# Kernel optimization log

Hardware: AMD Instinct MI355X
Metric: run time of the kernel (lower is better)

## Reference

```python
import jax, jax.numpy as jnp
import numpy as np

H = 12          # num heads
D = 768         # hidden size
DH = D // H     # size per head
FF = 3072       # intermediate size
EPS = 1e-11


def gelu(x):
    # tanh approximation, matching the TF source exactly
    c = np.sqrt(2.0 / np.pi).astype(np.float32)
    return x * 0.5 * (1.0 + jnp.tanh(c * (x + 0.044715 * jnp.power(x, 3))))


def layer_norm(x, gamma, beta):
    mean = jnp.mean(x, axis=-1, keepdims=True)
    var = jnp.mean(jnp.square(x - mean), axis=-1, keepdims=True)
    return (x - mean) * jax.lax.rsqrt(var + EPS) * gamma + beta


def setup_inputs() -> dict:
    key = jax.random.key(0)
    ks = jax.random.split(key, 12)
    B, S = 16, 512
    std = 0.02
    inp = {
        "x": jax.random.normal(ks[0], (B, S, D), jnp.float32),
        "mask": jnp.ones((B, S), dtype=bool),
        "Wq": jax.random.normal(ks[1], (D, D), jnp.float32) * std,
        "bq": jnp.zeros((D,), jnp.float32),
        "Wk": jax.random.normal(ks[2], (D, D), jnp.float32) * std,
        "bk": jnp.zeros((D,), jnp.float32),
        "Wv": jax.random.normal(ks[3], (D, D), jnp.float32) * std,
        "bv": jnp.zeros((D,), jnp.float32),
        "Wo": jax.random.normal(ks[4], (D, D), jnp.float32) * std,
        "bo": jnp.zeros((D,), jnp.float32),
        "g1": jnp.ones((D,), jnp.float32),
        "b1": jnp.zeros((D,), jnp.float32),
        "Wi": jax.random.normal(ks[5], (D, FF), jnp.float32) * std,
        "bi": jnp.zeros((FF,), jnp.float32),
        "Wo2": jax.random.normal(ks[6], (FF, D), jnp.float32) * std,
        "bo2": jnp.zeros((D,), jnp.float32),
        "g2": jnp.ones((D,), jnp.float32),
        "b2": jnp.zeros((D,), jnp.float32),
    }
    return inp


def reference(x, mask, Wq, bq, Wk, bk, Wv, bv, Wo, bo, g1, b1, Wi, bi, Wo2, bo2, g2, b2):
    B, S, _ = x.shape
    # QKV projections
    q = (x @ Wq + bq).reshape(B, S, H, DH)
    k = (x @ Wk + bk).reshape(B, S, H, DH)
    v = (x @ Wv + bv).reshape(B, S, H, DH)
    # scaled dot-product attention scores [B, H, S, S]
    scores = jnp.einsum("bqhd,bkhd->bhqk", q, k) / np.sqrt(DH).astype(np.float32)
    # key-side mask, applied as score * m + (1 - m) * -100 (per original source)
    m = mask[:, None, None, :].astype(jnp.float32)
    scores = scores * m + (1.0 - m) * (-100.0)
    probs = jax.nn.softmax(scores, axis=-1)
    attn = jnp.einsum("bhqk,bkhd->bqhd", probs, v).reshape(B, S, D)
    # tf.boolean_mask with all-True mask -> flatten batch and seq dims
    attn = attn.reshape(B * S, D)
    x_flat = x.reshape(B * S, D)
    # attention output projection + residual + LN
    attn_out = layer_norm(attn @ Wo + bo + x_flat, g1, b1)
    # FFN: gelu dense then output dense + residual + LN
    inter = gelu(attn_out @ Wi + bi)
    out = layer_norm(inter @ Wo2 + bo2 + attn_out, g2, b2)
    return out
```

## Files before the change

### kernel.cpp

```cpp
#include <hip/hip_runtime.h>


#define DEV __device__ __forceinline__

typedef unsigned short u16;
typedef unsigned int   u32;
typedef __bf16 bf16x8 __attribute__((ext_vector_type(8)));
typedef float  f32x4  __attribute__((ext_vector_type(4)));
typedef unsigned short u16x8 __attribute__((ext_vector_type(8)));
typedef unsigned short u16x4 __attribute__((ext_vector_type(4)));

DEV u16 f2bf(float f) {
    u32 u = __builtin_bit_cast(u32, f);
    u += 0x7fffu + ((u >> 16) & 1u);
    return (u16)(u >> 16);
}

DEV float gelu_f(float x) {
    float u = 0.7978845608028654f * (x + 0.044715f * x * x * x);
    float e = __expf(2.f * u);
    return 0.5f * x * (2.f - 2.f / (e + 1.f));
}

DEV void gload16(const void* gsrc, void* ldst) {
    __builtin_amdgcn_global_load_lds(
        (__attribute__((address_space(1))) void*)(void*)(const_cast<void*>(gsrc)),
        (__attribute__((address_space(3))) void*)ldst, 16, 0, 0);
}

DEV f32x4 MFMA(bf16x8 a, bf16x8 b, f32x4 c) {
    return __builtin_amdgcn_mfma_f32_16x16x32_bf16(a, b, c, 0, 0, 0);
}

__global__ __launch_bounds__(256) void cvt_bf16(const float* __restrict__ in,
                                                u16* __restrict__ out, int n) {
    int i = (blockIdx.x * 256 + threadIdx.x) * 4;
    if (i >= n) return;
    f32x4 v = *(const f32x4*)(in + i);
    u16x4 o;
    o.x = f2bf(v.x); o.y = f2bf(v.y); o.z = f2bf(v.z); o.w = f2bf(v.w);
    *(u16x4*)(out + i) = o;
}

__global__ __launch_bounds__(256) void transpose_cvt(const float* __restrict__ in,
                                                     u16* __restrict__ out,
                                                     int R, int C) {
    __shared__ float tile[32][33];
    int tx = threadIdx.x & 31, ty = threadIdx.x >> 5;
    int r0 = blockIdx.y * 32, c0 = blockIdx.x * 32;
#pragma unroll
    for (int i = 0; i < 4; i++)
        tile[ty + i * 8][tx] = in[(size_t)(r0 + ty + i * 8) * C + c0 + tx];
    __syncthreads();
#pragma unroll
    for (int i = 0; i < 4; i++)
        out[(size_t)(c0 + ty + i * 8) * R + r0 + tx] = f2bf(tile[tx][ty + i * 8]);
}

__global__ void concat_bias(const float* __restrict__ bq, const float* __restrict__ bk,
                            const float* __restrict__ bv, float* __restrict__ o) {
    int i = blockIdx.x * 256 + threadIdx.x;
    if (i < 2304) o[i] = (i < 768) ? bq[i] : (i < 1536 ? bk[i - 768] : bv[i - 1536]);
}

template <int EPI>
DEV void gemm_hi_body(const u16* __restrict__ A, const u16* __restrict__ BT,
                      const float* __restrict__ bias, void* __restrict__ Cout,
                      int N, int K, int ntn) {
    __shared__ __align__(16) char smem[32768];
    const int t = threadIdx.x, lane = t & 63, wid = t >> 6;
    const int nwg = gridDim.x, bid = blockIdx.x;
    const int swzb = ((nwg & 7) == 0) ? ((bid & 7) * (nwg >> 3) + (bid >> 3)) : bid;
    const int tm = swzb / ntn, tn = swzb % ntn;
    const int wm = wid >> 1, wn = wid & 1;

    f32x4 acc[4][4];
#pragma unroll
    for (int i = 0; i < 4; i++)
#pragma unroll
        for (int j = 0; j < 4; j++) acc[i][j] = f32x4{0.f, 0.f, 0.f, 0.f};

    const int NT = K >> 5;
    const u16* Ab = A + (size_t)tm * 128 * K;
    const u16* Bb = BT + (size_t)tn * 128 * K;

    int sr[2], sc[2];
#pragma unroll
    for (int j = 0; j < 2; j++) {
        int X = t * 16 + j * 4096;
        int Y = X ^ (((X >> 7) & 7) << 4);
        sr[j] = Y >> 6;
        sc[j] = (Y & 63) >> 1;
    }
    const u16* pA0 = Ab + (size_t)sr[0] * K + sc[0];
    const u16* pA1 = Ab + (size_t)sr[1] * K + sc[1];
    const u16* pB0 = Bb + (size_t)sr[0] * K + sc[0];
    const u16* pB1 = Bb + (size_t)sr[1] * K + sc[1];
    const int d0 = wid * 1024, d1 = wid * 1024 + 4096;

    const int g16 = (lane >> 4) << 4;
    const int rA = wm * 64 + (lane & 15);
    const int rB = wn * 64 + (lane & 15);
    const int aoff = (rA * 64 + g16) ^ (((rA >> 1) & 7) << 4);
    const int boff = 8192 + ((rB * 64 + g16) ^ (((rB >> 1) & 7) << 4));

#define STG(KT, BUF)                                                  \
    {                                                                 \
        char* s_ = smem + (BUF) * 16384;                              \
        gload16(pA0 + (KT), s_ + d0);                                 \
        gload16(pA1 + (KT), s_ + d1);                                 \
        gload16(pB0 + (KT), s_ + 8192 + d0);                          \
        gload16(pB1 + (KT), s_ + 8192 + d1);                          \
    }

    STG(0, 0);
    __syncthreads();

    for (int kt = 0; kt < NT; ++kt) {
        if (kt + 1 < NT) STG((kt + 1) << 5, (kt & 1) ^ 1);
        const char* buf = smem + (kt & 1) * 16384;
        bf16x8 af[4], bfr[4];
#pragma unroll
        for (int mi = 0; mi < 4; mi++) af[mi] = *(const bf16x8*)(buf + aoff + mi * 1024);
#pragma unroll
        for (int ni = 0; ni < 4; ni++) bfr[ni] = *(const bf16x8*)(buf + boff + ni * 1024);
        __builtin_amdgcn_s_setprio(1);
#pragma unroll
        for (int mi = 0; mi < 4; mi++)
#pragma unroll
            for (int ni = 0; ni < 4; ni++)
                acc[mi][ni] = MFMA(af[mi], bfr[ni], acc[mi][ni]);
        __builtin_amdgcn_s_setprio(0);
        __syncthreads();
    }
#undef STG

    const int r0 = tm * 128 + wm * 64, c0 = tn * 128 + wn * 64;
    float bcol[4];
#pragma unroll
    for (int ni = 0; ni < 4; ni++) bcol[ni] = bias[c0 + ni * 16 + (lane & 15)];
#pragma unroll
    for (int mi = 0; mi < 4; mi++) {
#pragma unroll
        for (int r = 0; r < 4; r++) {
            int gr = r0 + mi * 16 + ((lane >> 4) << 2) + r;
#pragma unroll
            for (int ni = 0; ni < 4; ni++) {
                int gc = c0 + ni * 16 + (lane & 15);
                float v = acc[mi][ni][r] + bcol[ni];
                if constexpr (EPI == 2) v = gelu_f(v);
                if constexpr (EPI == 1)
                    ((float*)Cout)[(size_t)gr * N + gc] = v;
                else
                    ((u16*)Cout)[(size_t)gr * N + gc] = f2bf(v);
            }
        }
    }
}

__global__ __launch_bounds__(256, 4) void gemm_qkv(const u16* __restrict__ A,
                                                   const u16* __restrict__ BT,
                                                   const float* __restrict__ bias,
                                                   void* __restrict__ Cout,
                                                   int N, int K, int ntn) {
    gemm_hi_body<0>(A, BT, bias, Cout, N, K, ntn);
}
__global__ __launch_bounds__(256, 4) void gemm_wo(const u16* __restrict__ A,
                                                  const u16* __restrict__ BT,
                                                  const float* __restrict__ bias,
                                                  void* __restrict__ Cout,
                                                  int N, int K, int ntn) {
    gemm_hi_body<1>(A, BT, bias, Cout, N, K, ntn);
}
__global__ __launch_bounds__(256, 4) void gemm_ffn1(const u16* __restrict__ A,
                                                    const u16* __restrict__ BT,
                                                    const float* __restrict__ bias,
                                                    void* __restrict__ Cout,
                                                    int N, int K, int ntn) {
    gemm_hi_body<2>(A, BT, bias, Cout, N, K, ntn);
}
__global__ __launch_bounds__(256, 4) void gemm_ffn2(const u16* __restrict__ A,
                                                    const u16* __restrict__ BT,
                                                    const float* __restrict__ bias,
                                                    void* __restrict__ Cout,
                                                    int N, int K, int ntn) {
    gemm_hi_body<1>(A, BT, bias, Cout, N, K, ntn);
}

__global__ __launch_bounds__(256) void attn_kernel(const u16* __restrict__ QKV,
                                                   u16* __restrict__ attnb) {
    __shared__ __align__(16) char sm[24576];
    char* Ks = sm;
    char* Vt = sm + 8192;
    const int t = threadIdx.x, lane = t & 63, wid = t >> 6;
    const int qt = blockIdx.x, bh = blockIdx.y;
    const int b = bh / 12, h = bh % 12;
    const size_t base = (size_t)b * 512 * 2304;
    char* Pw = sm + 16384 + wid * 2048;

    bf16x8 aq[2];
    {
        int qrow = qt * 64 + wid * 16 + (lane & 15);
        const u16* qp = QKV + base + (size_t)qrow * 2304 + h * 64 + ((lane >> 4) << 3);
        aq[0] = *(const bf16x8*)qp;
        aq[1] = *(const bf16x8*)(qp + 32);
    }
    f32x4 oacc[4];
#pragma unroll
    for (int g = 0; g < 4; g++) oacc[g] = f32x4{0.f, 0.f, 0.f, 0.f};
    float mrun[4] = {-1e30f, -1e30f, -1e30f, -1e30f};
    float lrun[4] = {0.f, 0.f, 0.f, 0.f};

    for (int kt = 0; kt < 8; ++kt) {
        __syncthreads();
#pragma unroll
        for (int i = 0; i < 2; i++) {
            int cw = wid * 2 + i;
            int o = cw * 1024 + lane * 16;
            int row = o >> 7;
            int cb = (o & 127) ^ ((row & 7) << 4);
            gload16(QKV + base + (size_t)(kt * 64 + row) * 2304 + 768 + h * 64 + (cb >> 1),
                    Ks + cw * 1024);
        }
        {
            int key = t & 63, dh0 = wid * 16;
            const u16* vp = QKV + base + (size_t)(kt * 64 + key) * 2304 + 1536 + h * 64 + dh0;
            u16x8 v0 = *(const u16x8*)vp;
            u16x8 v1 = *(const u16x8*)(vp + 8);
#pragma unroll
            for (int j = 0; j < 8; j++) {
                int dh = dh0 + j;
                *(u16*)(Vt + dh * 128 + ((key * 2) ^ ((dh & 7) << 4))) = v0[j];
            }
#pragma unroll
            for (int j = 0; j < 8; j++) {
                int dh = dh0 + 8 + j;
                *(u16*)(Vt + dh * 128 + ((key * 2) ^ ((dh & 7) << 4))) = v1[j];
            }
        }
        __syncthreads();

        f32x4 sacc[4];
#pragma unroll
        for (int ni = 0; ni < 4; ni++) sacc[ni] = f32x4{0.f, 0.f, 0.f, 0.f};
#pragma unroll
        for (int ni = 0; ni < 4; ni++) {
            int row = ni * 16 + (lane & 15);
#pragma unroll
            for (int ks = 0; ks < 2; ks++) {
                int cb = (ks * 64 + ((lane >> 4) << 4)) ^ ((row & 7) << 4);
                bf16x8 bk = *(const bf16x8*)(Ks + row * 128 + cb);
                sacc[ni] = MFMA(aq[ks], bk, sacc[ni]);
            }
        }
#pragma unroll
        for (int ni = 0; ni < 4; ni++)
#pragma unroll
            for (int r = 0; r < 4; r++) sacc[ni][r] *= 0.125f;

#pragma unroll
        for (int r = 0; r < 4; r++) {
            float pm = fmaxf(fmaxf(sacc[0][r], sacc[1][r]), fmaxf(sacc[2][r], sacc[3][r]));
            pm = fmaxf(pm, __shfl_xor(pm, 1));
            pm = fmaxf(pm, __shfl_xor(pm, 2));
            pm = fmaxf(pm, __shfl_xor(pm, 4));
            pm = fmaxf(pm, __shfl_xor(pm, 8));
            float mnew = fmaxf(mrun[r], pm);
            float sf = __expf(mrun[r] - mnew);
            mrun[r] = mnew;
            lrun[r] *= sf;
#pragma unroll
            for (int g = 0; g < 4; g++) oacc[g][r] *= sf;
            int prow = ((lane >> 4) << 2) + r;
            float ps = 0.f;
#pragma unroll
            for (int ni = 0; ni < 4; ni++) {
                float p = __expf(sacc[ni][r] - mnew);
                ps += p;
                int col = ni * 16 + (lane & 15);
                *(u16*)(Pw + prow * 128 + ((col * 2) ^ ((prow & 7) << 4))) = f2bf(p);
            }
            ps += __shfl_xor(ps, 1);
            ps += __shfl_xor(ps, 2);
            ps += __shfl_xor(ps, 4);
            ps += __shfl_xor(ps, 8);
            lrun[r] += ps;
        }
        __syncthreads();

#pragma unroll
        for (int ks = 0; ks < 2; ks++) {
            int prow = lane & 15;
            int pcb = (ks * 64 + ((lane >> 4) << 4)) ^ ((prow & 7) << 4);
            bf16x8 ap = *(const bf16x8*)(Pw + prow * 128 + pcb);
#pragma unroll
            for (int g = 0; g < 4; g++) {
                int vrow = g * 16 + (lane & 15);
                int vcb = (ks * 64 + ((lane >> 4) << 4)) ^ ((vrow & 7) << 4);
                bf16x8 bv = *(const bf16x8*)(Vt + vrow * 128 + vcb);
                oacc[g] = MFMA(ap, bv, oacc[g]);
            }
        }
    }

#pragma unroll
    for (int g = 0; g < 4; g++)
#pragma unroll
        for (int r = 0; r < 4; r++) {
            int qrow = qt * 64 + wid * 16 + ((lane >> 4) << 2) + r;
            float o = oacc[g][r] / lrun[r];
            attnb[(size_t)(b * 512 + qrow) * 768 + h * 64 + g * 16 + (lane & 15)] = f2bf(o);
        }
}

__global__ __launch_bounds__(256) void ln_kernel(const float* __restrict__ Y,
                                                 const float* __restrict__ res,
                                                 const float* __restrict__ g,
                                                 const float* __restrict__ bta,
                                                 float* __restrict__ outf,
                                                 u16* __restrict__ outb) {
    int row = blockIdx.x, t = threadIdx.x, lane = t & 63, wid = t >> 6;
    const float* y = Y + (size_t)row * 768;
    const float* rr = res + (size_t)row * 768;
    float v[3];
#pragma unroll
    for (int i = 0; i < 3; i++) v[i] = y[t + i * 256] + rr[t + i * 256];

    float s = v[0] + v[1] + v[2];
#pragma unroll
    for (int o = 32; o; o >>= 1) s += __shfl_xor(s, o);
    __shared__ float sm[4];
    __shared__ float bc[2];
    if (lane == 0) sm[wid] = s;
    __syncthreads();
    if (t == 0) bc[0] = (sm[0] + sm[1] + sm[2] + sm[3]) * (1.f / 768.f);
    __syncthreads();
    float mean = bc[0];

    float q = 0.f;
#pragma unroll
    for (int i = 0; i < 3; i++) { float d = v[i] - mean; q += d * d; }
#pragma unroll
    for (int o = 32; o; o >>= 1) q += __shfl_xor(q, o);
    if (lane == 0) sm[wid] = q;
    __syncthreads();
    if (t == 0) bc[1] = rsqrtf((sm[0] + sm[1] + sm[2] + sm[3]) * (1.f / 768.f) + 1e-11f);
    __syncthreads();
    float rs = bc[1];
#pragma unroll
    for (int i = 0; i < 3; i++) {
        int c = t + i * 256;
        float o = (v[i] - mean) * rs * g[c] + bta[c];
        outf[(size_t)row * 768 + c] = o;
        if (outb) outb[(size_t)row * 768 + c] = f2bf(o);
    }
}

extern "C" void kernel_launch(void* const* d_in, const int* in_sizes, int n_in,
                              void* d_out, int out_size, void* d_ws, size_t ws_size,
                              hipStream_t stream) {
    const float* x   = (const float*)d_in[0];
    const float* Wq  = (const float*)d_in[2];
    const float* bq  = (const float*)d_in[3];
    const float* Wk  = (const float*)d_in[4];
    const float* bk  = (const float*)d_in[5];
    const float* Wv  = (const float*)d_in[6];
    const float* bv  = (const float*)d_in[7];
    const float* Wo  = (const float*)d_in[8];
    const float* bo  = (const float*)d_in[9];
    const float* g1  = (const float*)d_in[10];
    const float* b1  = (const float*)d_in[11];
    const float* Wi  = (const float*)d_in[12];
    const float* bi  = (const float*)d_in[13];
    const float* Wo2 = (const float*)d_in[14];
    const float* bo2 = (const float*)d_in[15];
    const float* g2  = (const float*)d_in[16];
    const float* b2  = (const float*)d_in[17];

    char* w = (char*)d_ws;
    size_t off = 0;
    auto alloc = [&](size_t n) { size_t o = off; off += (n + 255) & ~(size_t)255; return o; };
    size_t oXb    = alloc((size_t)8192 * 768 * 2);
    size_t oWqkvT = alloc((size_t)2304 * 768 * 2);
    size_t oWoT   = alloc((size_t)768 * 768 * 2);
    size_t oWiT   = alloc((size_t)3072 * 768 * 2);
    size_t oWo2T  = alloc((size_t)768 * 3072 * 2);
    size_t oBqkv  = alloc((size_t)2304 * 4);
    size_t oR0    = alloc((size_t)8192 * 3072 * 2);
    size_t oY     = alloc((size_t)8192 * 768 * 4);
    size_t oAof   = alloc((size_t)8192 * 768 * 4);
    size_t oAob   = alloc((size_t)8192 * 768 * 2);
    (void)ws_size; (void)in_sizes; (void)n_in; (void)out_size;

    u16*   Xb    = (u16*)(w + oXb);
    u16*   WqkvT = (u16*)(w + oWqkvT);
    u16*   WoT   = (u16*)(w + oWoT);
    u16*   WiT   = (u16*)(w + oWiT);
    u16*   Wo2T  = (u16*)(w + oWo2T);
    float* bqkv  = (float*)(w + oBqkv);
    u16*   QKV   = (u16*)(w + oR0);
    u16*   attnb = (u16*)(w + oR0 + (size_t)8192 * 2304 * 2);
    u16*   inter = (u16*)(w + oR0);
    float* Y     = (float*)(w + oY);
    float* aof   = (float*)(w + oAof);
    u16*   aob   = (u16*)(w + oAob);

    cvt_bf16<<<6144, 256, 0, stream>>>(x, Xb, 8192 * 768);
    transpose_cvt<<<dim3(24, 24), 256, 0, stream>>>(Wq, WqkvT, 768, 768);
    transpose_cvt<<<dim3(24, 24), 256, 0, stream>>>(Wk, WqkvT + 768 * 768, 768, 768);
    transpose_cvt<<<dim3(24, 24), 256, 0, stream>>>(Wv, WqkvT + 2 * 768 * 768, 768, 768);
    transpose_cvt<<<dim3(24, 24), 256, 0, stream>>>(Wo, WoT, 768, 768);
    transpose_cvt<<<dim3(96, 24), 256, 0, stream>>>(Wi, WiT, 768, 3072);
    transpose_cvt<<<dim3(24, 96), 256, 0, stream>>>(Wo2, Wo2T, 3072, 768);
    concat_bias<<<9, 256, 0, stream>>>(bq, bk, bv, bqkv);

    gemm_qkv<<<1152, 256, 0, stream>>>(Xb, WqkvT, bqkv, QKV, 2304, 768, 18);
    attn_kernel<<<dim3(8, 192), 256, 0, stream>>>(QKV, attnb);
    gemm_wo<<<384, 256, 0, stream>>>(attnb, WoT, bo, Y, 768, 768, 6);
    ln_kernel<<<8192, 256, 0, stream>>>(Y, x, g1, b1, aof, aob);
    gemm_ffn1<<<1536, 256, 0, stream>>>(aob, WiT, bi, inter, 3072, 768, 24);
    gemm_ffn2<<<384, 256, 0, stream>>>(inter, Wo2T, bo2, Y, 768, 3072, 6);
    ln_kernel<<<8192, 256, 0, stream>>>(Y, aof, g2, b2, (float*)d_out, nullptr);
}
```

Baseline: 281.1 us.

## Triple-buffer GEMM pipeline, fuse prep kernels, store intermediates in bf16

The GEMM body moves from double to triple buffering of LDS tiles. It uses explicit vmcnt waits and raw barriers so two K-tiles stay in flight, and occupancy is lowered to 3 waves per SIMD for the extra LDS. The eight prep launches are merged into one kernel. The Wo/FFN2 outputs and the LN1 residual are now kept in bf16 instead of fp32, which cuts memory traffic but lowers precision in the residual path.

```diff
diff --git a/kernel.cpp b/kernel.cpp
--- a/kernel.cpp
+++ b/kernel.cpp
@@ -15,6 +15,7 @@
     u += 0x7fffu + ((u >> 16) & 1u);
     return (u16)(u >> 16);
 }
+DEV float bf2f(u16 u) { u32 x = (u32)u << 16; return __builtin_bit_cast(float, x); }
 
 DEV float gelu_f(float x) {
     float u = 0.7978845608028654f * (x + 0.044715f * x * x * x);
@@ -32,22 +33,49 @@
     return __builtin_amdgcn_mfma_f32_16x16x32_bf16(a, b, c, 0, 0, 0);
 }
 
-__global__ __launch_bounds__(256) void cvt_bf16(const float* __restrict__ in,
-                                                u16* __restrict__ out, int n) {
-    int i = (blockIdx.x * 256 + threadIdx.x) * 4;
-    if (i >= n) return;
-    f32x4 v = *(const f32x4*)(in + i);
-    u16x4 o;
-    o.x = f2bf(v.x); o.y = f2bf(v.y); o.z = f2bf(v.z); o.w = f2bf(v.w);
-    *(u16x4*)(out + i) = o;
-}
-
-__global__ __launch_bounds__(256) void transpose_cvt(const float* __restrict__ in,
-                                                     u16* __restrict__ out,
-                                                     int R, int C) {
+__global__ __launch_bounds__(256) void prep(
+    const float* __restrict__ x, const float* __restrict__ Wq,
+    const float* __restrict__ Wk, const float* __restrict__ Wv,
+    const float* __restrict__ Wo, const float* __restrict__ Wi,
+    const float* __restrict__ Wo2, const float* __restrict__ bq,
+    const float* __restrict__ bk, const float* __restrict__ bv,
+    u16* __restrict__ Xb, u16* __restrict__ WqkvT, u16* __restrict__ WoT,
+    u16* __restrict__ WiT, u16* __restrict__ Wo2T, float* __restrict__ bqkv) {
     __shared__ float tile[32][33];
-    int tx = threadIdx.x & 31, ty = threadIdx.x >> 5;
-    int r0 = blockIdx.y * 32, c0 = blockIdx.x * 32;
+    int bid = blockIdx.x, t = threadIdx.x;
+    if (bid < 6144) {
+        int i = (bid * 256 + t) * 4;
+        f32x4 v = *(const f32x4*)(x + i);
+        u16x4 o;
+        o.x = f2bf(v.x); o.y = f2bf(v.y); o.z = f2bf(v.z); o.w = f2bf(v.w);
+        *(u16x4*)(Xb + i) = o;
+        return;
+    }
+    bid -= 6144;
+    if (bid >= 6912) {
+        int i = (bid - 6912) * 256 + t;
+        if (i < 2304)
+            bqkv[i] = (i < 768) ? bq[i] : (i < 1536 ? bk[i - 768] : bv[i - 1536]);
+        return;
+    }
+    const float* in; u16* out; int R, C, bx, by;
+    if (bid < 1728) {
+        int w = bid / 576, idx = bid % 576;
+        in = (w == 0) ? Wq : (w == 1) ? Wk : Wv;
+        out = WqkvT + (size_t)w * 768 * 768;
+        R = 768; C = 768; bx = idx % 24; by = idx / 24;
+    } else if (bid < 2304) {
+        int idx = bid - 1728;
+        in = Wo; out = WoT; R = 768; C = 768; bx = idx % 24; by = idx / 24;
+    } else if (bid < 4608) {
+        int idx = bid - 2304;
+        in = Wi; out = WiT; R = 768; C = 3072; bx = idx % 96; by = idx / 96;
+    } else {
+        int idx = bid - 4608;
+        in = Wo2; out = Wo2T; R = 3072; C = 768; bx = idx % 24; by = idx / 24;
+    }
+    int tx = t & 31, ty = t >> 5;
+    int r0 = by * 32, c0 = bx * 32;
 #pragma unroll
     for (int i = 0; i < 4; i++)
         tile[ty + i * 8][tx] = in[(size_t)(r0 + ty + i * 8) * C + c0 + tx];
@@ -57,17 +85,11 @@
         out[(size_t)(c0 + ty + i * 8) * R + r0 + tx] = f2bf(tile[tx][ty + i * 8]);
 }
 
-__global__ void concat_bias(const float* __restrict__ bq, const float* __restrict__ bk,
-                            const float* __restrict__ bv, float* __restrict__ o) {
-    int i = blockIdx.x * 256 + threadIdx.x;
-    if (i < 2304) o[i] = (i < 768) ? bq[i] : (i < 1536 ? bk[i - 768] : bv[i - 1536]);
-}
-
 template <int EPI>
-DEV void gemm_hi_body(const u16* __restrict__ A, const u16* __restrict__ BT,
+DEV void gemm_c3_body(const u16* __restrict__ A, const u16* __restrict__ BT,
                       const float* __restrict__ bias, void* __restrict__ Cout,
                       int N, int K, int ntn) {
-    __shared__ __align__(16) char smem[32768];
+    __shared__ __align__(16) char smem[49152];
     const int t = threadIdx.x, lane = t & 63, wid = t >> 6;
     const int nwg = gridDim.x, bid = blockIdx.x;
     const int swzb = ((nwg & 7) == 0) ? ((bid & 7) * (nwg >> 3) + (bid >> 3)) : bid;
@@ -89,8 +111,7 @@
     for (int j = 0; j < 2; j++) {
         int X = t * 16 + j * 4096;
         int Y = X ^ (((X >> 7) & 7) << 4);
-        sr[j] = Y >> 6;
-        sc[j] = (Y & 63) >> 1;
+        sr[j] = Y >> 6; sc[j] = (Y & 63) >> 1;
     }
     const u16* pA0 = Ab + (size_t)sr[0] * K + sc[0];
     const u16* pA1 = Ab + (size_t)sr[1] * K + sc[1];
@@ -104,21 +125,24 @@
     const int aoff = (rA * 64 + g16) ^ (((rA >> 1) & 7) << 4);
     const int boff = 8192 + ((rB * 64 + g16) ^ (((rB >> 1) & 7) << 4));
 
-#define STG(KT, BUF)                                                  \
+#define STG(TT)                                                       \
     {                                                                 \
-        char* s_ = smem + (BUF) * 16384;                              \
-        gload16(pA0 + (KT), s_ + d0);                                 \
-        gload16(pA1 + (KT), s_ + d1);                                 \
-        gload16(pB0 + (KT), s_ + 8192 + d0);                          \
-        gload16(pB1 + (KT), s_ + 8192 + d1);                          \
-    }
-
-    STG(0, 0);
-    __syncthreads();
-
-    for (int kt = 0; kt < NT; ++kt) {
-        if (kt + 1 < NT) STG((kt + 1) << 5, (kt & 1) ^ 1);
-        const char* buf = smem + (kt & 1) * 16384;
+        char* s_ = smem + ((TT) % 3) * 16384;                         \
+        int ko_ = (TT) * 32;                                          \
+        gload16(pA0 + ko_, s_ + d0);                                  \
+        gload16(pA1 + ko_, s_ + d1);                                  \
+        gload16(pB0 + ko_, s_ + 8192 + d0);                           \
+        gload16(pB1 + ko_, s_ + 8192 + d1);                           \
+    }
+
+    STG(0) STG(1)
+    asm volatile("s_waitcnt vmcnt(4)" ::: "memory");
+    __builtin_amdgcn_s_barrier();
+    asm volatile("" ::: "memory");
+
+    for (int tt = 0; tt < NT; ++tt) {
+        if (tt + 2 < NT) STG(tt + 2)
+        const char* buf = smem + (tt % 3) * 16384;
         bf16x8 af[4], bfr[4];
 #pragma unroll
         for (int mi = 0; mi < 4; mi++) af[mi] = *(const bf16x8*)(buf + aoff + mi * 1024);
@@ -131,7 +155,12 @@
             for (int ni = 0; ni < 4; ni++)
                 acc[mi][ni] = MFMA(af[mi], bfr[ni], acc[mi][ni]);
         __builtin_amdgcn_s_setprio(0);
-        __syncthreads();
+        if (tt + 1 < NT) {
+            if (tt + 2 < NT) asm volatile("s_waitcnt vmcnt(4)" ::: "memory");
+            else             asm volatile("s_waitcnt vmcnt(0)" ::: "memory");
+        }
+        __builtin_amdgcn_s_barrier();
+        asm volatile("" ::: "memory");
     }
 #undef STG
 
@@ -149,42 +178,31 @@
                 int gc = c0 + ni * 16 + (lane & 15);
                 float v = acc[mi][ni][r] + bcol[ni];
                 if constexpr (EPI == 2) v = gelu_f(v);
-                if constexpr (EPI == 1)
-                    ((float*)Cout)[(size_t)gr * N + gc] = v;
-                else
-                    ((u16*)Cout)[(size_t)gr * N + gc] = f2bf(v);
-            }
-        }
-    }
-}
-
-__global__ __launch_bounds__(256, 4) void gemm_qkv(const u16* __restrict__ A,
-                                                   const u16* __restrict__ BT,
-                                                   const float* __restrict__ bias,
-                                                   void* __restrict__ Cout,
-                                                   int N, int K, int ntn) {
-    gemm_hi_body<0>(A, BT, bias, Cout, N, K, ntn);
-}
-__global__ __launch_bounds__(256, 4) void gemm_wo(const u16* __restrict__ A,
-                                                  const u16* __restrict__ BT,
-                                                  const float* __restrict__ bias,
-                                                  void* __restrict__ Cout,
+                ((u16*)Cout)[(size_t)gr * N + gc] = f2bf(v);
+            }
+        }
+    }
+}
+
+__global__ __launch_bounds__(256, 3) void g3_qkv(const u16* A, const u16* BT,
+                                                 const float* bias, void* C,
+                                                 int N, int K, int ntn) {
+    gemm_c3_body<0>(A, BT, bias, C, N, K, ntn);
+}
+__global__ __launch_bounds__(256, 3) void g3_wo(const u16* A, const u16* BT,
+                                                const float* bias, void* C,
+                                                int N, int K, int ntn) {
+    gemm_c3_body<0>(A, BT, bias, C, N, K, ntn);
+}
+__global__ __launch_bounds__(256, 3) void g3_ffn1(const u16* A, const u16* BT,
+                                                  const float* bias, void* C,
                                                   int N, int K, int ntn) {
-    gemm_hi_body<1>(A, BT, bias, Cout, N, K, ntn);
-}
-__global__ __launch_bounds__(256, 4) void gemm_ffn1(const u16* __restrict__ A,
-                                                    const u16* __restrict__ BT,
-                                                    const float* __restrict__ bias,
-                                                    void* __restrict__ Cout,
-                                                    int N, int K, int ntn) {
-    gemm_hi_body<2>(A, BT, bias, Cout, N, K, ntn);
-}
-__global__ __launch_bounds__(256, 4) void gemm_ffn2(const u16* __restrict__ A,
-                                                    const u16* __restrict__ BT,
-                                                    const float* __restrict__ bias,
-                                                    void* __restrict__ Cout,
-                                                    int N, int K, int ntn) {
-    gemm_hi_body<1>(A, BT, bias, Cout, N, K, ntn);
+    gemm_c3_body<2>(A, BT, bias, C, N, K, ntn);
+}
+__global__ __launch_bounds__(256, 3) void g3_ffn2(const u16* A, const u16* BT,
+                                                  const float* bias, void* C,
+                                                  int N, int K, int ntn) {
+    gemm_c3_body<0>(A, BT, bias, C, N, K, ntn);
 }
 
 __global__ __launch_bounds__(256) void attn_kernel(const u16* __restrict__ QKV,
@@ -313,18 +331,22 @@
         }
 }
 
-__global__ __launch_bounds__(256) void ln_kernel(const float* __restrict__ Y,
-                                                 const float* __restrict__ res,
-                                                 const float* __restrict__ g,
-                                                 const float* __restrict__ bta,
-                                                 float* __restrict__ outf,
-                                                 u16* __restrict__ outb) {
+template <int RESBF, int OUTF>
+__global__ __launch_bounds__(256) void ln_t(const u16* __restrict__ Yb,
+                                            const void* __restrict__ res,
+                                            const float* __restrict__ g,
+                                            const float* __restrict__ bta,
+                                            void* __restrict__ out) {
     int row = blockIdx.x, t = threadIdx.x, lane = t & 63, wid = t >> 6;
-    const float* y = Y + (size_t)row * 768;
-    const float* rr = res + (size_t)row * 768;
+    const u16* y = Yb + (size_t)row * 768;
     float v[3];
 #pragma unroll
-    for (int i = 0; i < 3; i++) v[i] = y[t + i * 256] + rr[t + i * 256];
+    for (int i = 0; i < 3; i++) {
+        int c = t + i * 256;
+        float rv = RESBF ? bf2f(((const u16*)res)[(size_t)row * 768 + c])
+                         : ((const float*)res)[(size_t)row * 768 + c];
+        v[i] = bf2f(y[c]) + rv;
+    }
 
     float s = v[0] + v[1] + v[2];
 #pragma unroll
@@ -351,8 +373,10 @@
     for (int i = 0; i < 3; i++) {
         int c = t + i * 256;
         float o = (v[i] - mean) * rs * g[c] + bta[c];
-        outf[(size_t)row * 768 + c] = o;
-        if (outb) outb[(size_t)row * 768 + c] = f2bf(o);
+        if constexpr (OUTF)
+            ((float*)out)[(size_t)row * 768 + c] = o;
+        else
+            ((u16*)out)[(size_t)row * 768 + c] = f2bf(o);
     }
 }
 
@@ -387,8 +411,7 @@
     size_t oWo2T  = alloc((size_t)768 * 3072 * 2);
     size_t oBqkv  = alloc((size_t)2304 * 4);
     size_t oR0    = alloc((size_t)8192 * 3072 * 2);
-    size_t oY     = alloc((size_t)8192 * 768 * 4);
-    size_t oAof   = alloc((size_t)8192 * 768 * 4);
+    size_t oYb    = alloc((size_t)8192 * 768 * 2);
     size_t oAob   = alloc((size_t)8192 * 768 * 2);
     (void)ws_size; (void)in_sizes; (void)n_in; (void)out_size;
 
@@ -401,24 +424,16 @@
     u16*   QKV   = (u16*)(w + oR0);
     u16*   attnb = (u16*)(w + oR0 + (size_t)8192 * 2304 * 2);
     u16*   inter = (u16*)(w + oR0);
-    float* Y     = (float*)(w + oY);
-    float* aof   = (float*)(w + oAof);
+    u16*   Yb    = (u16*)(w + oYb);
     u16*   aob   = (u16*)(w + oAob);
 
-    cvt_bf16<<<6144, 256, 0, stream>>>(x, Xb, 8192 * 768);
-    transpose_cvt<<<dim3(24, 24), 256, 0, stream>>>(Wq, WqkvT, 768, 768);
-    transpose_cvt<<<dim3(24, 24), 256, 0, stream>>>(Wk, WqkvT + 768 * 768, 768, 768);
-    transpose_cvt<<<dim3(24, 24), 256, 0, stream>>>(Wv, WqkvT + 2 * 768 * 768, 768, 768);
-    transpose_cvt<<<dim3(24, 24), 256, 0, stream>>>(Wo, WoT, 768, 768);
-    transpose_cvt<<<dim3(96, 24), 256, 0, stream>>>(Wi, WiT, 768, 3072);
-    transpose_cvt<<<dim3(24, 96), 256, 0, stream>>>(Wo2, Wo2T, 3072, 768);
-    concat_bias<<<9, 256, 0, stream>>>(bq, bk, bv, bqkv);
-
-    gemm_qkv<<<1152, 256, 0, stream>>>(Xb, WqkvT, bqkv, QKV, 2304, 768, 18);
+    prep<<<13065, 256, 0, stream>>>(x, Wq, Wk, Wv, Wo, Wi, Wo2, bq, bk, bv,
+                                    Xb, WqkvT, WoT, WiT, Wo2T, bqkv);
+    g3_qkv<<<1152, 256, 0, stream>>>(Xb, WqkvT, bqkv, QKV, 2304, 768, 18);
     attn_kernel<<<dim3(8, 192), 256, 0, stream>>>(QKV, attnb);
-    gemm_wo<<<384, 256, 0, stream>>>(attnb, WoT, bo, Y, 768, 768, 6);
-    ln_kernel<<<8192, 256, 0, stream>>>(Y, x, g1, b1, aof, aob);
-    gemm_ffn1<<<1536, 256, 0, stream>>>(aob, WiT, bi, inter, 3072, 768, 24);
-    gemm_ffn2<<<384, 256, 0, stream>>>(inter, Wo2T, bo2, Y, 768, 3072, 6);
-    ln_kernel<<<8192, 256, 0, stream>>>(Y, aof, g2, b2, (float*)d_out, nullptr);
-}
+    g3_wo<<<384, 256, 0, stream>>>(attnb, WoT, bo, Yb, 768, 768, 6);
+    ln_t<0, 0><<<8192, 256, 0, stream>>>(Yb, x, g1, b1, aob);
+    g3_ffn1<<<1536, 256, 0, stream>>>(aob, WiT, bi, inter, 3072, 768, 24);
+    g3_ffn2<<<384, 256, 0, stream>>>(inter, Wo2T, bo2, Yb, 768, 3072, 6);
+    ln_t<1, 1><<<8192, 256, 0, stream>>>(Yb, aob, g2, b2, (float*)d_out);
+}
```

New measurement: 257.7 us. 8.3% less time.
